# Kernel tuning notes

Hardware: AMD Instinct MI355X
Metric: run time of the kernel (lower is better)

The kernel has to match this reference:

```python
import jax, jax.numpy as jnp
import numpy as np

D_MODEL, D_FF, N_EXPERTS, TOP_K = 1024, 4096, 4, 2
B, S = 4, 2048


def setup_inputs() -> dict:
    key = jax.random.key(0)
    ks = jax.random.split(key, 7)
    s_r = 1.0 / np.sqrt(D_MODEL)
    s_f = 1.0 / np.sqrt(D_FF)
    return {
        "x": jax.random.normal(ks[0], (B, S, D_MODEL), dtype=jnp.float32),
        "Wr": jax.random.uniform(ks[1], (D_MODEL, N_EXPERTS), jnp.float32, -s_r, s_r),
        "br": jnp.zeros((N_EXPERTS,), jnp.float32),
        "W1": jax.random.uniform(ks[2], (N_EXPERTS, D_MODEL, D_FF), jnp.float32, -s_r, s_r),
        "b1": jax.random.uniform(ks[3], (N_EXPERTS, D_FF), jnp.float32, -s_r, s_r),
        "W2": jax.random.uniform(ks[4], (N_EXPERTS, D_FF, D_MODEL), jnp.float32, -s_f, s_f),
        "b2": jax.random.uniform(ks[5], (N_EXPERTS, D_MODEL), jnp.float32, -s_f, s_f),
    }


def reference(x, Wr, br, W1, b1, W2, b2):
    # Router: (B,S,E)
    router_logits = jnp.einsum("bsd,de->bse", x, Wr) + br
    router_probs = jax.nn.softmax(router_logits, axis=-1)
    top_k_probs, top_k_idx = jax.lax.top_k(router_probs, TOP_K)  # (B,S,K)
    top_k_probs = top_k_probs / jnp.sum(top_k_probs, axis=-1, keepdims=True)

    # Dense all-experts compute (faithful to original module).
    h = jnp.einsum("bsd,edf->bsef", x, W1) + b1          # (B,S,E,F)
    h = jax.nn.gelu(h, approximate=False)                 # torch nn.GELU (erf)
    expert_out = jnp.einsum("bsef,efd->bsed", h, W2) + b2  # (B,S,E,D)

    # Gather top-k expert outputs and combine with renormalized probs.
    sel = jnp.take_along_axis(expert_out, top_k_idx[..., None], axis=2)  # (B,S,K,D)
    out = jnp.sum(sel * top_k_probs[..., None], axis=2)   # (B,S,D)
    return out
```

## Files before the change

kernel.cpp:

```cpp
#include <hip/hip_runtime.h>
#include <hip/hip_bf16.h>
#include <hip/hip_fp16.h>
#include <stdint.h>

typedef float    f32x4 __attribute__((ext_vector_type(4)));
typedef float    fvec4 __attribute__((ext_vector_type(4)));
typedef _Float16 f16x8 __attribute__((ext_vector_type(8)));

#define D_MODEL 1024
#define D_FF    4096
#define NTOK    8192
#define CAP_ROWS 16896
#define NRB      132

#define OFF_W1  0UL
#define OFF_W2  33554432UL
#define OFF_XG  67108864UL
#define OFF_H   101711872UL
#define OFF_CNT 240123904UL
#define OFF_CUR 240123920UL
#define OFF_OFS 240123936UL
#define OFF_TOK 240124160UL
#define OFF_WGT 240191744UL
#define OFF_E12 240259328UL
#define OFF_W12 240292096UL
#define WS_NEED 240357632UL

__device__ __forceinline__ void gload_lds16(const void* g, void* l) {
  __builtin_amdgcn_global_load_lds(
      (const __attribute__((address_space(1))) unsigned int*)g,
      (__attribute__((address_space(3))) unsigned int*)l, 16, 0, 0);
}

__device__ __forceinline__ float fast_gelu(float v) {
  float v2 = v * v;
  float y2 = v * (2.302118131f + 0.10293924f * v2);
  float t = exp2f(y2);
  return v - v * __builtin_amdgcn_rcpf(1.f + t);
}

__device__ __forceinline__ void wtrans_body(
    const float* __restrict__ in, _Float16* __restrict__ out,
    int K, int N, int e, int n0, int k0, float (*tile)[65]) {
  const float* src = in + (size_t)e * K * N;
  _Float16* dst = out + (size_t)e * K * N;
  int t = threadIdx.x;
  {
    int kk = t >> 2, nc = (t & 3) * 16;
    const float* p = src + (size_t)(k0 + kk) * N + n0 + nc;
#pragma unroll
    for (int j = 0; j < 4; ++j) {
      fvec4 v = *(const fvec4*)(p + j * 4);
      tile[kk][nc + j * 4 + 0] = v[0]; tile[kk][nc + j * 4 + 1] = v[1];
      tile[kk][nc + j * 4 + 2] = v[2]; tile[kk][nc + j * 4 + 3] = v[3];
    }
  }
  __syncthreads();
  {
    int nn = t >> 2, kb = (t & 3) * 16;
    f16x8 o0, o1;
#pragma unroll
    for (int j = 0; j < 8; ++j) o0[j] = (_Float16)tile[kb + j][nn];
#pragma unroll
    for (int j = 0; j < 8; ++j) o1[j] = (_Float16)tile[kb + 8 + j][nn];
    _Float16* q = dst + (size_t)(n0 + nn) * K + k0 + kb;
    *(f16x8*)q = o0;
    *((f16x8*)q + 1) = o1;
  }
}

__global__ __launch_bounds__(256) void router_k(
    const float* __restrict__ x, const float* __restrict__ Wr,
    const float* __restrict__ br, int* __restrict__ e12,
    float* __restrict__ w12) {
  int wid = threadIdx.x >> 6, lane = threadIdx.x & 63;
  int t = blockIdx.x * 4 + wid;
  const float* xr = x + (size_t)t * D_MODEL;
  float a0 = 0.f, a1 = 0.f, a2 = 0.f, a3 = 0.f;
#pragma unroll
  for (int c = 0; c < 4; ++c) {
    int d0 = c * 256 + lane * 4;
    fvec4 xv = *(const fvec4*)(xr + d0);
#pragma unroll
    for (int j = 0; j < 4; ++j) {
      fvec4 wv = *(const fvec4*)(Wr + (size_t)(d0 + j) * 4);
      a0 += xv[j] * wv[0]; a1 += xv[j] * wv[1];
      a2 += xv[j] * wv[2]; a3 += xv[j] * wv[3];
    }
  }
#pragma unroll
  for (int m = 32; m; m >>= 1) {
    a0 += __shfl_xor(a0, m, 64); a1 += __shfl_xor(a1, m, 64);
    a2 += __shfl_xor(a2, m, 64); a3 += __shfl_xor(a3, m, 64);
  }
  if (lane == 0) {
    float l[4] = {a0 + br[0], a1 + br[1], a2 + br[2], a3 + br[3]};
    int e1 = 0; float m1 = l[0];
#pragma unroll
    for (int e = 1; e < 4; ++e) if (l[e] > m1) { m1 = l[e]; e1 = e; }
    int e2 = -1; float m2 = -1e30f;
#pragma unroll
    for (int e = 0; e < 4; ++e) if (e != e1 && l[e] > m2) { m2 = l[e]; e2 = e; }
    float tt = expf(m2 - m1);
    float w1 = 1.f / (1.f + tt), w2 = tt / (1.f + tt);
    e12[t] = e1 | (e2 << 8);
    w12[2 * t] = w1; w12[2 * t + 1] = w2;
  }
}

__global__ __launch_bounds__(256) void plan_k(
    int* __restrict__ e12, const float* __restrict__ w12,
    int* __restrict__ counts, int* __restrict__ offs,
    int* __restrict__ tok) {
  __shared__ int ls[4][256];
  __shared__ int lt[4];
  __shared__ int lo[5];
  int tid = threadIdx.x;
  int t0 = tid * 32;
  int pe[32];
  int c0 = 0, c1 = 0, c2 = 0, c3 = 0;
#pragma unroll
  for (int j = 0; j < 32; ++j) {
    int p = e12[t0 + j];
    pe[j] = p;
    int e1 = p & 255, e2 = p >> 8;
    c0 += (e1 == 0) + (e2 == 0);
    c1 += (e1 == 1) + (e2 == 1);
    c2 += (e1 == 2) + (e2 == 2);
    c3 += (e1 == 3) + (e2 == 3);
  }
  ls[0][tid] = c0; ls[1][tid] = c1; ls[2][tid] = c2; ls[3][tid] = c3;
  __syncthreads();
  int wv = tid >> 6, lane = tid & 63;
  {
    int s0 = ls[wv][lane * 4 + 0], s1 = ls[wv][lane * 4 + 1];
    int s2 = ls[wv][lane * 4 + 2], s3 = ls[wv][lane * 4 + 3];
    int s = s0 + s1 + s2 + s3;
    int incl = s;
#pragma unroll
    for (int d = 1; d < 64; d <<= 1) {
      int tsh = __shfl_up(incl, d, 64);
      if (lane >= d) incl += tsh;
    }
    int excl = incl - s;
    ls[wv][lane * 4 + 0] = excl;
    ls[wv][lane * 4 + 1] = excl + s0;
    ls[wv][lane * 4 + 2] = excl + s0 + s1;
    ls[wv][lane * 4 + 3] = excl + s0 + s1 + s2;
    if (lane == 63) lt[wv] = incl;
  }
  __syncthreads();
  if (tid == 0) {
    int o = 0;
#pragma unroll
    for (int e = 0; e < 4; ++e) {
      lo[e] = o; offs[e] = o; counts[e] = lt[e];
      o += (lt[e] + 127) & ~127;
    }
    lo[4] = o; offs[4] = o;
  }
  __syncthreads();
  int b0 = lo[0] + ls[0][tid], b1 = lo[1] + ls[1][tid];
  int b2 = lo[2] + ls[2][tid], b3 = lo[3] + ls[3][tid];
#pragma unroll
  for (int j = 0; j < 32; ++j) {
    int p = pe[j];
    int t = t0 + j;
    int e1 = p & 255, e2 = p >> 8;
    int s1 = (e1 == 0) ? b0 : (e1 == 1) ? b1 : (e1 == 2) ? b2 : b3;
    tok[s1] = t;
    b0 += (e1 == 0); b1 += (e1 == 1); b2 += (e1 == 2); b3 += (e1 == 3);
    int s2 = (e2 == 0) ? b0 : (e2 == 1) ? b1 : (e2 == 2) ? b2 : b3;
    tok[s2] = t;
    b0 += (e2 == 0); b1 += (e2 == 1); b2 += (e2 == 2); b3 += (e2 == 3);
    e12[t] = s1 | (s2 << 16);
  }
}

__global__ __launch_bounds__(256) void gatherw_k(
    const float* __restrict__ x, const int* __restrict__ offs,
    const int* __restrict__ counts, const int* __restrict__ tok,
    _Float16* __restrict__ Xg,
    const float* __restrict__ W1, _Float16* __restrict__ W1f) {
  __shared__ float tile[64][65];
  int b = blockIdx.x;
  if (b >= 8448) {
    int bb = b - 8448;
    int n0 = (bb & 63) * 64, k0 = ((bb >> 6) & 15) * 64, e = bb >> 10;
    wtrans_body(W1, W1f, 1024, 4096, e, n0, k0, tile);
    return;
  }
  int row = b * 2 + (threadIdx.x >> 7);
  int tid = threadIdx.x & 127;
  if (row >= offs[4]) return;
  int e = 0;
  while (e < 3 && row >= offs[e + 1]) ++e;
  f16x8 o;
  if (row < offs[e] + counts[e]) {
    int t = tok[row];
    const float* src = x + (size_t)t * D_MODEL + tid * 8;
    fvec4 v0 = *(const fvec4*)src;
    fvec4 v1 = *(const fvec4*)(src + 4);
#pragma unroll
    for (int j = 0; j < 4; ++j) { o[j] = (_Float16)v0[j]; o[4 + j] = (_Float16)v1[j]; }
  } else {
#pragma unroll
    for (int j = 0; j < 8; ++j) o[j] = (_Float16)0.f;
  }
  *(f16x8*)(Xg + (size_t)row * D_MODEL + tid * 8) = o;
}

__device__ __forceinline__ f16x8 lds_frag(const char* base, int row, int kbyte) {
  return *(const f16x8*)(base + row * 128 + (kbyte ^ ((row & 7) << 4)));
}

__global__ __launch_bounds__(256, 2) void gemm1x_k(
    const _Float16* __restrict__ A, const _Float16* __restrict__ B,
    const float* __restrict__ bias, const int* __restrict__ offs,
    const int* __restrict__ counts, _Float16* __restrict__ outH,
    const float* __restrict__ W2, _Float16* __restrict__ W2f) {
  __shared__ char lds[49152];
  int bid = blockIdx.x;
  if (bid >= 2112) {
    int bb = bid - 2112;
    int n0 = (bb & 15) * 64, k0 = ((bb >> 4) & 63) * 64, e = bb >> 10;
    wtrans_body(W2, W2f, 4096, 1024, e, n0, k0, (float(*)[65])lds);
    return;
  }
  int wg = (bid & 7) * 264 + (bid >> 3);
  int col = wg & 15, row = wg >> 4;
  int rowBase = row * 128;
  if (rowBase >= offs[4]) return;
  int e = 0;
  while (e < 3 && rowBase >= offs[e + 1]) ++e;
  if (rowBase >= offs[e] + counts[e]) return;
  int colBase = col * 256;

  int tid = threadIdx.x, wid = tid >> 6, lane = tid & 63;
  int wr = wid >> 1, wc = wid & 1;
  int ln = lane & 15;
  int srow = lane >> 3;
  int kx = (lane & 7) ^ srow;
  const _Float16* Abase = A + (size_t)rowBase * 1024 + kx * 8;
  const _Float16* Bbase = B + (size_t)e * D_FF * 1024 + (size_t)colBase * 1024 + kx * 8;
  char* ldsA = lds;
  char* ldsB = lds + 16384;

  f32x4 acc[4][8];
  f32x4 zero = {0.f, 0.f, 0.f, 0.f};
#pragma unroll
  for (int m = 0; m < 4; ++m)
#pragma unroll
    for (int n = 0; n < 8; ++n) acc[m][n] = zero;

  for (int k0 = 0; k0 < 1024; k0 += 64) {
#pragma unroll
    for (int i = 0; i < 4; ++i) {
      int chunk = wid * 4 + i;
      gload_lds16(Abase + (size_t)(chunk * 8 + srow) * 1024 + k0, ldsA + chunk * 1024);
    }
#pragma unroll
    for (int i = 0; i < 8; ++i) {
      int chunk = wid * 8 + i;
      gload_lds16(Bbase + (size_t)(chunk * 8 + srow) * 1024 + k0, ldsB + chunk * 1024);
    }
    __syncthreads();
#pragma unroll
    for (int kk = 0; kk < 2; ++kk) {
      int kbyte = kk * 64 + (lane >> 4) * 16;
      f16x8 af[4], bf[8];
#pragma unroll
      for (int m = 0; m < 4; ++m)
        af[m] = lds_frag(ldsA, wr * 64 + m * 16 + ln, kbyte);
#pragma unroll
      for (int n = 0; n < 8; ++n)
        bf[n] = lds_frag(ldsB, wc * 128 + n * 16 + ln, kbyte);
#pragma unroll
      for (int m = 0; m < 4; ++m)
#pragma unroll
        for (int n = 0; n < 8; ++n)
          acc[m][n] = __builtin_amdgcn_mfma_f32_16x16x32_f16(af[m], bf[n], acc[m][n], 0, 0, 0);
    }
    __syncthreads();
  }

  int col0 = colBase + wc * 128 + ln;
  float bv[8];
#pragma unroll
  for (int n = 0; n < 8; ++n) bv[n] = bias[(size_t)e * D_FF + col0 + n * 16];
#pragma unroll
  for (int m = 0; m < 4; ++m) {
    int rbase = rowBase + wr * 64 + m * 16 + (lane >> 4) * 4;
#pragma unroll
    for (int j = 0; j < 4; ++j) {
      size_t ro = (size_t)(rbase + j) * D_FF;
#pragma unroll
      for (int n = 0; n < 8; ++n) {
        float v = fast_gelu(acc[m][n][j] + bv[n]);
        outH[ro + col0 + n * 16] = (_Float16)v;
      }
    }
  }
}

__global__ __launch_bounds__(256, 4) void gemm2_k(
    const _Float16* __restrict__ A, const _Float16* __restrict__ B,
    const float* __restrict__ bias, const int* __restrict__ offs,
    const int* __restrict__ counts, _Float16* __restrict__ Eout) {
  __shared__ char lds[32768];
  int bid = blockIdx.x;
  int wg = (bid & 7) * 132 + (bid >> 3);
  int col = wg & 7, row = wg >> 3;
  int rowBase = row * 128;
  if (rowBase >= offs[4]) return;
  int e = 0;
  while (e < 3 && rowBase >= offs[e + 1]) ++e;
  int eoff = offs[e], cnt = counts[e];
  if (rowBase >= eoff + cnt) return;
  int colBase = col * 128;

  int tid = threadIdx.x, wid = tid >> 6, lane = tid & 63;
  int wr = wid >> 1, wc = wid & 1;
  int ln = lane & 15;
  int srow = lane >> 3;
  int kx = (lane & 7) ^ srow;
  const _Float16* Abase = A + (size_t)rowBase * 4096 + kx * 8;
  const _Float16* Bbase = B + (size_t)e * D_MODEL * 4096 + (size_t)colBase * 4096 + kx * 8;
  char* ldsA = lds;
  char* ldsB = lds + 16384;

  f32x4 acc[4][4];
  f32x4 zero = {0.f, 0.f, 0.f, 0.f};
#pragma unroll
  for (int m = 0; m < 4; ++m)
#pragma unroll
    for (int n = 0; n < 4; ++n) acc[m][n] = zero;

  for (int k0 = 0; k0 < 4096; k0 += 64) {
#pragma unroll
    for (int i = 0; i < 4; ++i) {
      int chunk = wid * 4 + i;
      gload_lds16(Abase + (size_t)(chunk * 8 + srow) * 4096 + k0, ldsA + chunk * 1024);
      gload_lds16(Bbase + (size_t)(chunk * 8 + srow) * 4096 + k0, ldsB + chunk * 1024);
    }
    __syncthreads();
#pragma unroll
    for (int kk = 0; kk < 2; ++kk) {
      int kbyte = kk * 64 + (lane >> 4) * 16;
      f16x8 af[4], bf[4];
#pragma unroll
      for (int m = 0; m < 4; ++m)
        af[m] = lds_frag(ldsA, wr * 64 + m * 16 + ln, kbyte);
#pragma unroll
      for (int n = 0; n < 4; ++n)
        bf[n] = lds_frag(ldsB, wc * 64 + n * 16 + ln, kbyte);
#pragma unroll
      for (int m = 0; m < 4; ++m)
#pragma unroll
        for (int n = 0; n < 4; ++n)
          acc[m][n] = __builtin_amdgcn_mfma_f32_16x16x32_f16(af[m], bf[n], acc[m][n], 0, 0, 0);
    }
    __syncthreads();
  }

  int col0 = colBase + wc * 64 + ln;
  float bv[4];
#pragma unroll
  for (int n = 0; n < 4; ++n) bv[n] = bias[(size_t)e * D_MODEL + col0 + n * 16];
#pragma unroll
  for (int m = 0; m < 4; ++m) {
    int rbase = rowBase + wr * 64 + m * 16 + (lane >> 4) * 4;
#pragma unroll
    for (int j = 0; j < 4; ++j) {
      int grow = rbase + j;
      if (grow - eoff < cnt) {
        size_t o = (size_t)grow * D_MODEL + col0;
#pragma unroll
        for (int n = 0; n < 4; ++n)
          Eout[o + n * 16] = (_Float16)(acc[m][n][j] + bv[n]);
      }
    }
  }
}

__global__ __launch_bounds__(256) void combine_k(
    const _Float16* __restrict__ Eout, const int* __restrict__ sl12,
    const float* __restrict__ w12, float* __restrict__ out) {
  int t = blockIdx.x * 2 + (threadIdx.x >> 7);
  int tid = threadIdx.x & 127;
  int p = sl12[t];
  int s1 = p & 0xffff, s2 = (p >> 16) & 0xffff;
  float w1 = w12[2 * t], w2 = w12[2 * t + 1];
  f16x8 a = *(const f16x8*)(Eout + (size_t)s1 * D_MODEL + tid * 8);
  f16x8 b = *(const f16x8*)(Eout + (size_t)s2 * D_MODEL + tid * 8);
  fvec4 o0, o1;
#pragma unroll
  for (int j = 0; j < 4; ++j) {
    o0[j] = w1 * (float)a[j] + w2 * (float)b[j];
    o1[j] = w1 * (float)a[4 + j] + w2 * (float)b[4 + j];
  }
  float* dst = out + (size_t)t * D_MODEL + tid * 8;
  *(fvec4*)dst = o0;
  *(fvec4*)(dst + 4) = o1;
}

extern "C" void kernel_launch(void* const* d_in, const int* in_sizes, int n_in,
                              void* d_out, int out_size, void* d_ws, size_t ws_size,
                              hipStream_t stream) {
  const float* x  = (const float*)d_in[0];
  const float* Wr = (const float*)d_in[1];
  const float* br = (const float*)d_in[2];
  const float* W1 = (const float*)d_in[3];
  const float* b1 = (const float*)d_in[4];
  const float* W2 = (const float*)d_in[5];
  const float* b2 = (const float*)d_in[6];
  float* out = (float*)d_out;
  char* ws = (char*)d_ws;
  if (ws_size < WS_NEED) return;

  _Float16* W1f = (_Float16*)(ws + OFF_W1);
  _Float16* W2f = (_Float16*)(ws + OFF_W2);
  _Float16* Xg  = (_Float16*)(ws + OFF_XG);
  _Float16* H   = (_Float16*)(ws + OFF_H);
  int*   counts = (int*)(ws + OFF_CNT);
  int*   offs   = (int*)(ws + OFF_OFS);
  int*   tok    = (int*)(ws + OFF_TOK);
  int*   e12    = (int*)(ws + OFF_E12);
  float* w12    = (float*)(ws + OFF_W12);

  router_k<<<NTOK / 4, 256, 0, stream>>>(x, Wr, br, e12, w12);
  plan_k<<<1, 256, 0, stream>>>(e12, w12, counts, offs, tok);
  gatherw_k<<<12544, 256, 0, stream>>>(x, offs, counts, tok, Xg, W1, W1f);
  gemm1x_k<<<6208, 256, 0, stream>>>(Xg, W1f, b1, offs, counts, H, W2, W2f);
  gemm2_k<<<NRB * 8, 256, 0, stream>>>(H, W2f, b2, offs, counts, Xg);
  combine_k<<<NTOK / 2, 256, 0, stream>>>(Xg, e12, w12, out);
}
```

Baseline: 457.9 us.

## Fuse token gather into GEMM1 A-loads and merge fp16 cast into router kernel

The separate gather kernel that wrote a padded, expert-sorted fp16 copy of the activations is removed. The router kernel now also converts all of x to fp16 densely and performs the W1 transpose. GEMM1 then loads A rows indirectly through the token index table. The plan kernel zero-fills the padding token slots so padded rows read a valid row, and expert outputs reuse the x16 buffer. This drops one launch and a full write and read of the padded gather buffer, at the cost of per-row indirect, less sequential A loads inside the GEMM.

Result: faster. 446.0 us (-2.6%).

```diff
diff --git a/kernel.cpp b/kernel.cpp
--- a/kernel.cpp
+++ b/kernel.cpp
@@ -18,10 +18,8 @@
 #define OFF_XG  67108864UL
 #define OFF_H   101711872UL
 #define OFF_CNT 240123904UL
-#define OFF_CUR 240123920UL
 #define OFF_OFS 240123936UL
 #define OFF_TOK 240124160UL
-#define OFF_WGT 240191744UL
 #define OFF_E12 240259328UL
 #define OFF_W12 240292096UL
 #define WS_NEED 240357632UL
@@ -69,12 +67,34 @@
   }
 }
 
-__global__ __launch_bounds__(256) void router_k(
+__global__ __launch_bounds__(256) void rwc_k(
     const float* __restrict__ x, const float* __restrict__ Wr,
     const float* __restrict__ br, int* __restrict__ e12,
-    float* __restrict__ w12) {
+    float* __restrict__ w12,
+    const float* __restrict__ W1, _Float16* __restrict__ W1f,
+    _Float16* __restrict__ x16) {
+  __shared__ float tile[64][65];
+  int b = blockIdx.x;
+  if (b >= 6144) {
+    int row = (b - 6144) * 2 + (threadIdx.x >> 7);
+    int tid = threadIdx.x & 127;
+    const float* src = x + (size_t)row * D_MODEL + tid * 8;
+    fvec4 v0 = *(const fvec4*)src;
+    fvec4 v1 = *(const fvec4*)(src + 4);
+    f16x8 o;
+#pragma unroll
+    for (int j = 0; j < 4; ++j) { o[j] = (_Float16)v0[j]; o[4 + j] = (_Float16)v1[j]; }
+    *(f16x8*)(x16 + (size_t)row * D_MODEL + tid * 8) = o;
+    return;
+  }
+  if (b >= 2048) {
+    int bb = b - 2048;
+    int n0 = (bb & 63) * 64, k0 = ((bb >> 6) & 15) * 64, e = bb >> 10;
+    wtrans_body(W1, W1f, 1024, 4096, e, n0, k0, tile);
+    return;
+  }
   int wid = threadIdx.x >> 6, lane = threadIdx.x & 63;
-  int t = blockIdx.x * 4 + wid;
+  int t = b * 4 + wid;
   const float* xr = x + (size_t)t * D_MODEL;
   float a0 = 0.f, a1 = 0.f, a2 = 0.f, a3 = 0.f;
 #pragma unroll
@@ -175,39 +195,12 @@
     b0 += (e2 == 0); b1 += (e2 == 1); b2 += (e2 == 2); b3 += (e2 == 3);
     e12[t] = s1 | (s2 << 16);
   }
-}
-
-__global__ __launch_bounds__(256) void gatherw_k(
-    const float* __restrict__ x, const int* __restrict__ offs,
-    const int* __restrict__ counts, const int* __restrict__ tok,
-    _Float16* __restrict__ Xg,
-    const float* __restrict__ W1, _Float16* __restrict__ W1f) {
-  __shared__ float tile[64][65];
-  int b = blockIdx.x;
-  if (b >= 8448) {
-    int bb = b - 8448;
-    int n0 = (bb & 63) * 64, k0 = ((bb >> 6) & 15) * 64, e = bb >> 10;
-    wtrans_body(W1, W1f, 1024, 4096, e, n0, k0, tile);
-    return;
-  }
-  int row = b * 2 + (threadIdx.x >> 7);
-  int tid = threadIdx.x & 127;
-  if (row >= offs[4]) return;
-  int e = 0;
-  while (e < 3 && row >= offs[e + 1]) ++e;
-  f16x8 o;
-  if (row < offs[e] + counts[e]) {
-    int t = tok[row];
-    const float* src = x + (size_t)t * D_MODEL + tid * 8;
-    fvec4 v0 = *(const fvec4*)src;
-    fvec4 v1 = *(const fvec4*)(src + 4);
-#pragma unroll
-    for (int j = 0; j < 4; ++j) { o[j] = (_Float16)v0[j]; o[4 + j] = (_Float16)v1[j]; }
-  } else {
-#pragma unroll
-    for (int j = 0; j < 8; ++j) o[j] = (_Float16)0.f;
-  }
-  *(f16x8*)(Xg + (size_t)row * D_MODEL + tid * 8) = o;
+#pragma unroll
+  for (int e = 0; e < 4; ++e) {
+    int start = lo[e] + lt[e];
+    int end = lo[e + 1];
+    for (int i = start + tid; i < end; i += 256) tok[i] = 0;
+  }
 }
 
 __device__ __forceinline__ f16x8 lds_frag(const char* base, int row, int kbyte) {
@@ -215,9 +208,10 @@
 }
 
 __global__ __launch_bounds__(256, 2) void gemm1x_k(
-    const _Float16* __restrict__ A, const _Float16* __restrict__ B,
+    const _Float16* __restrict__ x16, const _Float16* __restrict__ B,
     const float* __restrict__ bias, const int* __restrict__ offs,
-    const int* __restrict__ counts, _Float16* __restrict__ outH,
+    const int* __restrict__ counts, const int* __restrict__ tok,
+    _Float16* __restrict__ outH,
     const float* __restrict__ W2, _Float16* __restrict__ W2f) {
   __shared__ char lds[49152];
   int bid = blockIdx.x;
@@ -241,7 +235,12 @@
   int ln = lane & 15;
   int srow = lane >> 3;
   int kx = (lane & 7) ^ srow;
-  const _Float16* Abase = A + (size_t)rowBase * 1024 + kx * 8;
+  const _Float16* Asrc[4];
+#pragma unroll
+  for (int i = 0; i < 4; ++i) {
+    int tk = tok[rowBase + (wid * 4 + i) * 8 + srow];
+    Asrc[i] = x16 + (size_t)tk * 1024 + kx * 8;
+  }
   const _Float16* Bbase = B + (size_t)e * D_FF * 1024 + (size_t)colBase * 1024 + kx * 8;
   char* ldsA = lds;
   char* ldsB = lds + 16384;
@@ -257,7 +256,7 @@
 #pragma unroll
     for (int i = 0; i < 4; ++i) {
       int chunk = wid * 4 + i;
-      gload_lds16(Abase + (size_t)(chunk * 8 + srow) * 1024 + k0, ldsA + chunk * 1024);
+      gload_lds16(Asrc[i] + k0, ldsA + chunk * 1024);
     }
 #pragma unroll
     for (int i = 0; i < 8; ++i) {
@@ -420,18 +419,18 @@
 
   _Float16* W1f = (_Float16*)(ws + OFF_W1);
   _Float16* W2f = (_Float16*)(ws + OFF_W2);
-  _Float16* Xg  = (_Float16*)(ws + OFF_XG);
+  _Float16* x16 = (_Float16*)(ws + OFF_XG);
   _Float16* H   = (_Float16*)(ws + OFF_H);
   int*   counts = (int*)(ws + OFF_CNT);
   int*   offs   = (int*)(ws + OFF_OFS);
   int*   tok    = (int*)(ws + OFF_TOK);
   int*   e12    = (int*)(ws + OFF_E12);
   float* w12    = (float*)(ws + OFF_W12);
-
-  router_k<<<NTOK / 4, 256, 0, stream>>>(x, Wr, br, e12, w12);
+  _Float16* Eout = x16;
+
+  rwc_k<<<10240, 256, 0, stream>>>(x, Wr, br, e12, w12, W1, W1f, x16);
   plan_k<<<1, 256, 0, stream>>>(e12, w12, counts, offs, tok);
-  gatherw_k<<<12544, 256, 0, stream>>>(x, offs, counts, tok, Xg, W1, W1f);
-  gemm1x_k<<<6208, 256, 0, stream>>>(Xg, W1f, b1, offs, counts, H, W2, W2f);
-  gemm2_k<<<NRB * 8, 256, 0, stream>>>(H, W2f, b2, offs, counts, Xg);
-  combine_k<<<NTOK / 2, 256, 0, stream>>>(Xg, e12, w12, out);
-}
+  gemm1x_k<<<6208, 256, 0, stream>>>(x16, W1f, b1, offs, counts, tok, H, W2, W2f);
+  gemm2_k<<<NRB * 8, 256, 0, stream>>>(H, W2f, b2, offs, counts, Eout);
+  combine_k<<<NTOK / 2, 256, 0, stream>>>(Eout, e12, w12, out);
+}
```
